# Performance work log

Hardware: AMD Instinct MI355X
Metric: run time of the kernel (lower is better)

The kernel has to match this reference:

```python
import jax, jax.numpy as jnp
import numpy as np

N1, N2, D = 8192, 8192, 8

def setup_inputs() -> dict:
    key = jax.random.key(0)
    k1, k2 = jax.random.split(key)
    input1 = jax.random.uniform(k1, (N1, D), dtype=jnp.float32)
    input2 = jax.random.uniform(k2, (N2, D), dtype=jnp.float32)
    gamma = jnp.array(1.0, dtype=jnp.float32)
    return {"input1": input1, "input2": input2, "gamma": gamma}

def reference(input1, input2, gamma):
    # array[i, j] = exp((sum_d (input1[i,d] - input2[j,d]))**2) * gamma
    # sum_d (x_i - c_j) = rowsum(x)_i - rowsum(c)_j, so reduce first then broadcast.
    s1 = jnp.sum(input1, axis=1)  # (N1,)
    s2 = jnp.sum(input2, axis=1)  # (N2,)
    diff = s1[:, None] - s2[None, :]  # (N1, N2)
    return jnp.exp(diff * diff) * gamma
```

## Files before the change

### kernel.cpp

```cpp
#include <hip/hip_runtime.h>

#define N1 8192
#define N2 8192
#define D  8

__global__ void rbf_rowsum_kernel(const float* __restrict__ in1,
                                  const float* __restrict__ in2,
                                  float* __restrict__ s) {
    int idx = blockIdx.x * blockDim.x + threadIdx.x;
    if (idx < N1) {
        const float4* p = reinterpret_cast<const float4*>(in1 + (size_t)idx * D);
        float4 a = p[0];
        float4 b = p[1];
        s[idx] = ((a.x + a.y) + (a.z + a.w)) + ((b.x + b.y) + (b.z + b.w));
    } else if (idx < N1 + N2) {
        int j = idx - N1;
        const float4* p = reinterpret_cast<const float4*>(in2 + (size_t)j * D);
        float4 a = p[0];
        float4 b = p[1];
        s[N1 + j] = ((a.x + a.y) + (a.z + a.w)) + ((b.x + b.y) + (b.z + b.w));
    }
}

__global__ void __launch_bounds__(256)
rbf_main_kernel(const float* __restrict__ s,
                const float* __restrict__ gamma_p,
                float4* __restrict__ out) {
    const int i  = blockIdx.y;
    const int j4 = blockIdx.x * blockDim.x + threadIdx.x;

    const float s1i = s[i];
    const float g   = gamma_p[0];

    const float4 s2v = reinterpret_cast<const float4*>(s + N1)[j4];

    float4 r;
    {
        float d0 = s1i - s2v.x;
        float d1 = s1i - s2v.y;
        float d2 = s1i - s2v.z;
        float d3 = s1i - s2v.w;
        r.x = __expf(d0 * d0) * g;
        r.y = __expf(d1 * d1) * g;
        r.z = __expf(d2 * d2) * g;
        r.w = __expf(d3 * d3) * g;
    }

    out[(size_t)i * (N2 / 4) + j4] = r;
}

extern "C" void kernel_launch(void* const* d_in, const int* in_sizes, int n_in,
                              void* d_out, int out_size, void* d_ws, size_t ws_size,
                              hipStream_t stream) {
    const float* in1     = (const float*)d_in[0];
    const float* in2     = (const float*)d_in[1];
    const float* gamma_p = (const float*)d_in[2];
    float* ws  = (float*)d_ws;
    float4* out = (float4*)d_out;

    {
        const int threads = 256;
        const int total   = N1 + N2;
        const int blocks  = (total + threads - 1) / threads;
        rbf_rowsum_kernel<<<blocks, threads, 0, stream>>>(in1, in2, ws);
    }

    {
        dim3 block(256);
        dim3 grid(N2 / (256 * 4), N1);
        rbf_main_kernel<<<grid, block, 0, stream>>>(ws, gamma_p, out);
    }
}
```

Before: 48.56 us.

## Fuse rowsum into main kernel with 32-row tiles and nontemporal stores

Merges the row-sum pre-pass into the output kernel. Each block computes its input2 column sums in registers and its input1 row sums into shared memory, then writes 32 output rows per thread block using nontemporal stores. This removes one kernel launch and the workspace round trip, and spreads the per-block setup cost over 32 rows. The trade-off is that input2 row sums are recomputed by every row-block, and each thread's own rowsum loads are strided across memory.

```diff
diff --git a/kernel.cpp b/kernel.cpp
--- a/kernel.cpp
+++ b/kernel.cpp
@@ -1,52 +1,60 @@
 #include <hip/hip_runtime.h>
+
 
 #define N1 8192
 #define N2 8192
 #define D  8
+#define ROWS 32
 
-__global__ void rbf_rowsum_kernel(const float* __restrict__ in1,
-                                  const float* __restrict__ in2,
-                                  float* __restrict__ s) {
-    int idx = blockIdx.x * blockDim.x + threadIdx.x;
-    if (idx < N1) {
-        const float4* p = reinterpret_cast<const float4*>(in1 + (size_t)idx * D);
-        float4 a = p[0];
-        float4 b = p[1];
-        s[idx] = ((a.x + a.y) + (a.z + a.w)) + ((b.x + b.y) + (b.z + b.w));
-    } else if (idx < N1 + N2) {
-        int j = idx - N1;
-        const float4* p = reinterpret_cast<const float4*>(in2 + (size_t)j * D);
-        float4 a = p[0];
-        float4 b = p[1];
-        s[N1 + j] = ((a.x + a.y) + (a.z + a.w)) + ((b.x + b.y) + (b.z + b.w));
-    }
+typedef float f32x4 __attribute__((ext_vector_type(4)));
+
+__device__ __forceinline__ float rowsum8(const float* __restrict__ p) {
+    const f32x4* q = reinterpret_cast<const f32x4*>(p);
+    f32x4 a = q[0];
+    f32x4 b = q[1];
+    return ((a.x + a.y) + (a.z + a.w)) + ((b.x + b.y) + (b.z + b.w));
 }
 
 __global__ void __launch_bounds__(256)
-rbf_main_kernel(const float* __restrict__ s,
-                const float* __restrict__ gamma_p,
-                float4* __restrict__ out) {
-    const int i  = blockIdx.y;
-    const int j4 = blockIdx.x * blockDim.x + threadIdx.x;
+rbf_fused_kernel(const float* __restrict__ in1,
+                 const float* __restrict__ in2,
+                 const float* __restrict__ gamma_p,
+                 f32x4* __restrict__ out) {
+    const int cb = blockIdx.x;
+    const int rb = blockIdx.y;
+    const int t  = threadIdx.x;
 
-    const float s1i = s[i];
-    const float g   = gamma_p[0];
+    __shared__ float s1s[ROWS];
 
-    const float4 s2v = reinterpret_cast<const float4*>(s + N1)[j4];
+    const int col0 = cb * 1024 + t * 4;
+    float s20 = rowsum8(in2 + (size_t)(col0 + 0) * D);
+    float s21 = rowsum8(in2 + (size_t)(col0 + 1) * D);
+    float s22 = rowsum8(in2 + (size_t)(col0 + 2) * D);
+    float s23 = rowsum8(in2 + (size_t)(col0 + 3) * D);
 
-    float4 r;
-    {
-        float d0 = s1i - s2v.x;
-        float d1 = s1i - s2v.y;
-        float d2 = s1i - s2v.z;
-        float d3 = s1i - s2v.w;
-        r.x = __expf(d0 * d0) * g;
-        r.y = __expf(d1 * d1) * g;
-        r.z = __expf(d2 * d2) * g;
-        r.w = __expf(d3 * d3) * g;
+    if (t < ROWS) {
+        s1s[t] = rowsum8(in1 + (size_t)(rb * ROWS + t) * D);
     }
+    const float g = gamma_p[0];
+    __syncthreads();
 
-    out[(size_t)i * (N2 / 4) + j4] = r;
+    f32x4* __restrict__ orow = out + (size_t)(rb * ROWS) * (N2 / 4) + cb * 256 + t;
+
+    #pragma unroll 4
+    for (int r = 0; r < ROWS; ++r) {
+        const float s1 = s1s[r];
+        float d0 = s1 - s20;
+        float d1 = s1 - s21;
+        float d2 = s1 - s22;
+        float d3 = s1 - s23;
+        f32x4 v;
+        v.x = __expf(d0 * d0) * g;
+        v.y = __expf(d1 * d1) * g;
+        v.z = __expf(d2 * d2) * g;
+        v.w = __expf(d3 * d3) * g;
+        __builtin_nontemporal_store(v, orow);
+        orow += N2 / 4;
+    }
 }
 
 extern "C" void kernel_launch(void* const* d_in, const int* in_sizes, int n_in,
@@ -55,19 +63,9 @@
     const float* in1     = (const float*)d_in[0];
     const float* in2     = (const float*)d_in[1];
     const float* gamma_p = (const float*)d_in[2];
-    float* ws  = (float*)d_ws;
-    float4* out = (float4*)d_out;
+    f32x4* out = (f32x4*)d_out;
 
-    {
-        const int threads = 256;
-        const int total   = N1 + N2;
-        const int blocks  = (total + threads - 1) / threads;
-        rbf_rowsum_kernel<<<blocks, threads, 0, stream>>>(in1, in2, ws);
-    }
-
-    {
-        dim3 block(256);
-        dim3 grid(N2 / (256 * 4), N1);
-        rbf_main_kernel<<<grid, block, 0, stream>>>(ws, gamma_p, out);
-    }
+    dim3 block(256);
+    dim3 grid(N2 / 1024, N1 / ROWS);
+    rbf_fused_kernel<<<grid, block, 0, stream>>>(in1, in2, gamma_p, out);
 }
```

New measurement: 49.05 us, median of 2. No clear change (+1.0%).
